# Kernel tuning notes

Hardware: AMD Instinct MI355X
Metric: run time of the kernel (lower is better)

Reference implementation:

```python
import jax, jax.numpy as jnp
import numpy as np

N = 8192
IN_DIM = 512
HID = 512


def setup_inputs() -> dict:
    key = jax.random.key(0)
    k1, k2, k3, k4 = jax.random.split(key, 4)
    input_features = jax.random.normal(k1, (N, IN_DIM), dtype=jnp.float32)
    # positive weighted adjacency so degrees > 0
    adjacency_matrix = jax.random.uniform(k2, (N, N), dtype=jnp.float32)
    # xavier_init: normal with std = 1/sqrt(in_dim/2)
    Wgcn1 = jax.random.normal(k3, (IN_DIM, HID), dtype=jnp.float32) * (1.0 / np.sqrt(IN_DIM / 2.0))
    bgcn1 = jnp.zeros((HID,), dtype=jnp.float32)
    Wgcn12 = jax.random.normal(k4, (HID, HID), dtype=jnp.float32) * (1.0 / np.sqrt(HID / 2.0))
    bgcn12 = jnp.zeros((HID,), dtype=jnp.float32)
    return {
        "input_features": input_features,
        "adjacency_matrix": adjacency_matrix,
        "Wgcn1": Wgcn1,
        "bgcn1": bgcn1,
        "Wgcn12": Wgcn12,
        "bgcn12": bgcn12,
    }


def reference(input_features, adjacency_matrix, Wgcn1, bgcn1, Wgcn12, bgcn12):
    # D^{-1/2} A D^{-1/2}: diag matmuls expressed as row/col elementwise scaling
    # (mathematically identical to torch.matmul(diag(d), A @ diag(d)))
    d_inv_sqrt = jnp.power(adjacency_matrix.sum(axis=1), -0.5)  # [N]
    norm_adj = d_inv_sqrt[:, None] * adjacency_matrix * d_inv_sqrt[None, :]  # [N, N]

    support = input_features @ Wgcn1            # [N, HID]
    out = norm_adj @ support + bgcn1            # [N, HID]
    out = jax.nn.relu(out)                      # dropout p=0.0 -> identity
    support = out @ Wgcn12                      # [N, HID]
    out = norm_adj @ support + bgcn12           # [N, HID]
    return out
```

## Files before the change

### kernel.cpp

```cpp
#include <hip/hip_runtime.h>
#include <stdint.h>


typedef __attribute__((ext_vector_type(8))) __bf16 bf16x8;
typedef __attribute__((ext_vector_type(4))) float f32x4;
typedef __attribute__((ext_vector_type(8))) unsigned short u16x8;

__device__ __forceinline__ unsigned short f2bf(float f) {
  union { float f; uint32_t u; } v; v.f = f;
  uint32_t u = v.u;
  return (unsigned short)((u + 0x7fffu + ((u >> 16) & 1u)) >> 16);
}

__device__ __forceinline__ float bf2f(unsigned short u) {
  union { uint32_t u; float f; } v; v.u = ((uint32_t)u) << 16; return v.f;
}

__device__ __forceinline__ void async_cp16(const void* g, void* lds) {
  auto gp = (const __attribute__((address_space(1))) uint32_t*)g;
  auto lp = (__attribute__((address_space(3))) uint32_t*)lds;
  __builtin_amdgcn_global_load_lds(gp, lp, 16, 0, 0);
}

__global__ __launch_bounds__(256) void k_rowsum_convert(
    const float* __restrict__ A, unsigned short* __restrict__ Abf,
    float* __restrict__ dvec, int ncols) {
  const int row = blockIdx.x;
  const float* arow = A + (size_t)row * ncols;
  unsigned short* orow = Abf + (size_t)row * ncols;
  float s = 0.f;
  for (int c = threadIdx.x * 4; c < ncols; c += 256 * 4) {
    float4 v = *(const float4*)(arow + c);
    s += (v.x + v.y) + (v.z + v.w);
    ushort4 o;
    o.x = f2bf(v.x); o.y = f2bf(v.y); o.z = f2bf(v.z); o.w = f2bf(v.w);
    *(ushort4*)(orow + c) = o;
  }
  #pragma unroll
  for (int off = 32; off > 0; off >>= 1) s += __shfl_down(s, off);
  __shared__ float red[4];
  if ((threadIdx.x & 63) == 0) red[threadIdx.x >> 6] = s;
  __syncthreads();
  if (threadIdx.x == 0) {
    float t = (red[0] + red[1]) + (red[2] + red[3]);
    dvec[row] = 1.0f / sqrtf(t);
  }
}

__global__ __launch_bounds__(256) void k_f32_to_bf16(
    const float* __restrict__ in, unsigned short* __restrict__ out, int n4) {
  int i = blockIdx.x * 256 + threadIdx.x;
  if (i < n4) {
    float4 v = ((const float4*)in)[i];
    ushort4 o;
    o.x = f2bf(v.x); o.y = f2bf(v.y); o.z = f2bf(v.z); o.w = f2bf(v.w);
    ((ushort4*)out)[i] = o;
  }
}

__global__ __launch_bounds__(256) void k_transpose_bf16(
    const float* __restrict__ in, unsigned short* __restrict__ out, int dim) {
  int o = blockIdx.x * 256 + threadIdx.x;
  if (o < dim * dim) {
    int k = o % dim;
    int n = o / dim;
    out[o] = f2bf(in[k * dim + n]);
  }
}

template <int MODE>
__global__ __launch_bounds__(256, 2) void gemm_bt(
    const unsigned short* __restrict__ Aop,
    const unsigned short* __restrict__ Bt,
    void* __restrict__ Cout,
    const float* __restrict__ dvec,
    const float* __restrict__ bias,
    int M, int N, int K) {
  constexpr int BM = 128, BN = 64, BK = 32;
  __shared__ unsigned short As[BM * BK];
  __shared__ unsigned short Bs[BN * BK];

  const int tid = threadIdx.x;
  const int w = tid >> 6;
  const int l = tid & 63;
  const int rowBase = blockIdx.y * BM;
  const int colBase = blockIdx.x * BN;
  const int waveM = w >> 1;
  const int waveN = w & 1;

  f32x4 acc[4][2];
  const f32x4 fz = {0.f, 0.f, 0.f, 0.f};
  #pragma unroll
  for (int m = 0; m < 4; ++m)
    #pragma unroll
    for (int n = 0; n < 2; ++n) acc[m][n] = fz;

  const int chunkRow = l >> 2;
  const int kOff = (l & 3) * 8;
  const unsigned short* gA0 = Aop + (size_t)(rowBase + w * 16 + chunkRow) * K + kOff;
  const unsigned short* gA1 = gA0 + (size_t)64 * K;
  const unsigned short* gB0 = Bt + (size_t)(colBase + w * 16 + chunkRow) * K + kOff;
  unsigned short* lA0 = As + w * 512;
  unsigned short* lA1 = As + (w + 4) * 512;
  unsigned short* lB0 = Bs + w * 512;

  const int kfrag = (l >> 4) * 8;
  const int lrow = l & 15;

  for (int k0 = 0; k0 < K; k0 += BK) {
    async_cp16(gA0 + k0, lA0);
    async_cp16(gA1 + k0, lA1);
    async_cp16(gB0 + k0, lB0);
    __syncthreads();

    bf16x8 af[4], bfr[2];
    #pragma unroll
    for (int m = 0; m < 4; ++m)
      af[m] = *(const bf16x8*)(As + (waveM * 64 + m * 16 + lrow) * BK + kfrag);
    #pragma unroll
    for (int n = 0; n < 2; ++n)
      bfr[n] = *(const bf16x8*)(Bs + (waveN * 32 + n * 16 + lrow) * BK + kfrag);

    #pragma unroll
    for (int m = 0; m < 4; ++m)
      #pragma unroll
      for (int n = 0; n < 2; ++n)
        acc[m][n] = __builtin_amdgcn_mfma_f32_16x16x32_bf16(af[m], bfr[n],
                                                            acc[m][n], 0, 0, 0);
    __syncthreads();
  }

  const int erow0 = rowBase + waveM * 64 + (l >> 4) * 4;
  const int ecol0 = colBase + waveN * 32 + (l & 15);
  #pragma unroll
  for (int m = 0; m < 4; ++m) {
    #pragma unroll
    for (int n = 0; n < 2; ++n) {
      #pragma unroll
      for (int j = 0; j < 4; ++j) {
        const int rowg = erow0 + m * 16 + j;
        const int colg = ecol0 + n * 16;
        float v = acc[m][n][j];
        if (MODE == 0) {
          v *= dvec[colg];
          ((unsigned short*)Cout)[(size_t)rowg * N + colg] = f2bf(v);
        }
      }
    }
  }
}

__global__ __launch_bounds__(512, 1) void gemm_big3(
    const unsigned short* __restrict__ Aop,
    const unsigned short* __restrict__ Bt,
    unsigned short* __restrict__ Pout,
    int M, int N, int K, int kLen) {
  constexpr int BK = 32;
  __shared__ char lds[3 * 32768];

  const int tid = threadIdx.x;
  const int w = tid >> 6;
  const int l = tid & 63;

  const int id = blockIdx.x;
  const int q = id & 7, s = id >> 3;
  const int bx = s & 1;
  const int by = ((q & 1) << 4) | (s >> 1);
  const int bz = q >> 1;

  const int rowBase = by * 256;
  const int colBase = bx * 256;
  const int kBase = bz * kLen;
  const int waveM = w >> 2;
  const int waveN = w & 3;

  f32x4 acc[8][4];
  const f32x4 fz = {0.f, 0.f, 0.f, 0.f};
  #pragma unroll
  for (int m = 0; m < 8; ++m)
    #pragma unroll
    for (int n = 0; n < 4; ++n) acc[m][n] = fz;

  const int srcElem = ((l & 3) ^ ((l >> 3) & 3)) * 8;
  const unsigned short* aSrc =
      Aop + (size_t)(rowBase + w * 32 + (l >> 2)) * K + kBase + srcElem;
  const unsigned short* bSrc =
      Bt + (size_t)(colBase + w * 32 + (l >> 2)) * K + kBase + srcElem;
  const int dstTh = w * 2048 + l * 16;

#define STAGE_A(tt, bb)                                                   \
  {                                                                       \
    const size_t o = (size_t)(tt) * BK;                                   \
    async_cp16(aSrc + o, lds + (bb) + dstTh);                             \
    async_cp16(aSrc + (size_t)16 * K + o, lds + (bb) + dstTh + 1024);     \
  }
#define STAGE_B(tt, bb)                                                   \
  {                                                                       \
    const size_t o = (size_t)(tt) * BK;                                   \
    async_cp16(bSrc + o, lds + (bb) + 16384 + dstTh);                     \
    async_cp16(bSrc + (size_t)16 * K + o, lds + (bb) + 16384 + dstTh + 1024); \
  }

  const int nt = kLen / BK;
  STAGE_A(0, 0); STAGE_B(0, 0);
  STAGE_A(1, 32768); STAGE_B(1, 32768);

  const int lrow = l & 15;
  const int kq = l >> 4;
  const int xr = (lrow >> 1) & 3;
  const int slotByte = ((kq ^ xr) << 4);
  const int aRow0 = (waveM * 128 + lrow) * 64;
  const int bRow0 = 16384 + (waveN * 64 + lrow) * 64;

  int cur = 0, nxt = 32768, fut = 65536;
  for (int t = 0; t < nt; ++t) {
    if (t == nt - 1) {
      asm volatile("s_waitcnt vmcnt(0)" ::: "memory");
    } else {
      asm volatile("s_waitcnt vmcnt(4)" ::: "memory");
    }
    __builtin_amdgcn_s_barrier();

    bf16x8 af[4], bfr[4];
    #pragma unroll
    for (int i = 0; i < 4; ++i)
      af[i] = *(const bf16x8*)(lds + cur + aRow0 + i * 16 * 64 + slotByte);
    #pragma unroll
    for (int n = 0; n < 4; ++n)
      bfr[n] = *(const bf16x8*)(lds + cur + bRow0 + n * 16 * 64 + slotByte);
    if (t + 2 < nt) STAGE_A(t + 2, fut);
    __builtin_amdgcn_s_barrier();
    __builtin_amdgcn_s_setprio(1);
    #pragma unroll
    for (int i = 0; i < 4; ++i)
      #pragma unroll
      for (int n = 0; n < 4; ++n)
        acc[i][n] = __builtin_amdgcn_mfma_f32_16x16x32_bf16(
            af[i], bfr[n], acc[i][n], 0, 0, 0);
    __builtin_amdgcn_s_setprio(0);

    bf16x8 af2[4];
    #pragma unroll
    for (int i = 0; i < 4; ++i)
      af2[i] = *(const bf16x8*)(lds + cur + aRow0 + (64 + i * 16) * 64 + slotByte);
    if (t + 2 < nt) STAGE_B(t + 2, fut);
    __builtin_amdgcn_s_barrier();
    __builtin_amdgcn_s_setprio(1);
    #pragma unroll
    for (int i = 0; i < 4; ++i)
      #pragma unroll
      for (int n = 0; n < 4; ++n)
        acc[4 + i][n] = __builtin_amdgcn_mfma_f32_16x16x32_bf16(
            af2[i], bfr[n], acc[4 + i][n], 0, 0, 0);
    __builtin_amdgcn_s_setprio(0);

    const int tmp = cur; cur = nxt; nxt = fut; fut = tmp;
  }
#undef STAGE_A
#undef STAGE_B

  unsigned short* pz = Pout + (size_t)bz * M * N;
  const int erow0 = rowBase + waveM * 128 + (l >> 4) * 4;
  const int ecol0 = colBase + waveN * 64 + (l & 15);
  #pragma unroll
  for (int m = 0; m < 8; ++m) {
    #pragma unroll
    for (int n = 0; n < 4; ++n) {
      #pragma unroll
      for (int j = 0; j < 4; ++j) {
        pz[(size_t)(erow0 + m * 16 + j) * N + ecol0 + n * 16] =
            f2bf(acc[m][n][j]);
      }
    }
  }
}

template <int MODE>
__global__ __launch_bounds__(256) void k_reduce(
    const unsigned short* __restrict__ parts,
    const float* __restrict__ dvec,
    const float* __restrict__ bias,
    void* __restrict__ outp, int M, int N) {
  const size_t MN = (size_t)M * N;
  const size_t idx = ((size_t)blockIdx.x * 256 + threadIdx.x) * 8;
  if (idx >= MN) return;
  const int row = (int)(idx / N);
  const int col = (int)(idx % N);
  const float di = dvec[row];
  float s[8] = {0, 0, 0, 0, 0, 0, 0, 0};
  #pragma unroll
  for (int z = 0; z < 4; ++z) {
    u16x8 v = *(const u16x8*)(parts + z * MN + idx);
    #pragma unroll
    for (int e = 0; e < 8; ++e) s[e] += bf2f(v[e]);
  }
  if (MODE == 1) {
    ushort4 o0, o1;
    unsigned short tmp[8];
    #pragma unroll
    for (int e = 0; e < 8; ++e) {
      float v = di * s[e] + bias[col + e];
      v = v > 0.f ? v : 0.f;
      tmp[e] = f2bf(v);
    }
    o0.x = tmp[0]; o0.y = tmp[1]; o0.z = tmp[2]; o0.w = tmp[3];
    o1.x = tmp[4]; o1.y = tmp[5]; o1.z = tmp[6]; o1.w = tmp[7];
    *(ushort4*)((unsigned short*)outp + idx) = o0;
    *(ushort4*)((unsigned short*)outp + idx + 4) = o1;
  } else {
    float4 o0, o1;
    o0.x = di * s[0] + bias[col + 0];
    o0.y = di * s[1] + bias[col + 1];
    o0.z = di * s[2] + bias[col + 2];
    o0.w = di * s[3] + bias[col + 3];
    o1.x = di * s[4] + bias[col + 4];
    o1.y = di * s[5] + bias[col + 5];
    o1.z = di * s[6] + bias[col + 6];
    o1.w = di * s[7] + bias[col + 7];
    *(float4*)((float*)outp + idx) = o0;
    *(float4*)((float*)outp + idx + 4) = o1;
  }
}

extern "C" void kernel_launch(void* const* d_in, const int* in_sizes, int n_in,
                              void* d_out, int out_size, void* d_ws, size_t ws_size,
                              hipStream_t stream) {
  const float* X  = (const float*)d_in[0];
  const float* A  = (const float*)d_in[1];
  const float* W1 = (const float*)d_in[2];
  const float* b1 = (const float*)d_in[3];
  const float* W2 = (const float*)d_in[4];
  const float* b2 = (const float*)d_in[5];
  float* out = (float*)d_out;

  constexpr int NN = 8192, IN = 512, HID = 512;
  constexpr int KSPLIT = 4;

  char* ws = (char*)d_ws;
  float* ddeg = (float*)ws;
  unsigned short* Abf = (unsigned short*)(ws + (32 << 10));
  unsigned short* W1t = Abf + (size_t)NN * NN;
  unsigned short* W2t = W1t + IN * HID;
  unsigned short* P0  = W2t + HID * HID;
  unsigned short* P1  = P0 + (size_t)NN * HID;
  unsigned short* parts = P1 + (size_t)NN * HID;

  k_rowsum_convert<<<NN, 256, 0, stream>>>(A, Abf, ddeg, NN);
  k_f32_to_bf16<<<(NN * IN / 4 + 255) / 256, 256, 0, stream>>>(X, P0, NN * IN / 4);
  k_transpose_bf16<<<(IN * HID + 255) / 256, 256, 0, stream>>>(W1, W1t, IN);
  k_transpose_bf16<<<(HID * HID + 255) / 256, 256, 0, stream>>>(W2, W2t, HID);

  gemm_bt<0><<<dim3(NN / 64, HID / 128), 256, 0, stream>>>(
      W1t, P0, P1, ddeg, nullptr, HID, NN, IN);
  gemm_big3<<<2 * (NN / 256) * KSPLIT, 512, 0, stream>>>(
      Abf, P1, parts, NN, HID, NN, NN / KSPLIT);
  k_reduce<1><<<(int)((size_t)NN * HID / 8 / 256), 256, 0, stream>>>(
      parts, ddeg, b1, P0, NN, HID);
  gemm_bt<0><<<dim3(NN / 64, HID / 128), 256, 0, stream>>>(
      W2t, P0, P1, ddeg, nullptr, HID, NN, HID);
  gemm_big3<<<2 * (NN / 256) * KSPLIT, 512, 0, stream>>>(
      Abf, P1, parts, NN, HID, NN, NN / KSPLIT);
  k_reduce<2><<<(int)((size_t)NN * HID / 8 / 256), 256, 0, stream>>>(
      parts, ddeg, b2, out, NN, HID);
}
```

Measured before the change: 263.3 us.

## Rewrite big GEMM mainloop with BK=64 double buffer and phased staggered prefetch

Replaces the triple-buffered BK=32 main loop of the split-K adjacency GEMM with a double-buffered BK=64 loop using 128 KB LDS and an 8-way XOR swizzle. Each K-tile is split into four MFMA phases separated by barriers. The A and B prefetches are staggered so A for the next tile and B for the tile after next are issued across different phases. The aim is to halve the barrier and wait overhead per unit of K and overlap global-to-LDS copies with MFMA work. In exchange it adds more barriers per iteration and depends on fragile vmcnt accounting. The launch bound also changes to 2, while 128 KB of LDS per block still likely allows only one block per CU.

```diff
diff --git a/kernel.cpp b/kernel.cpp
--- a/kernel.cpp
+++ b/kernel.cpp
@@ -150,13 +150,12 @@
   }
 }
 
-__global__ __launch_bounds__(512, 1) void gemm_big3(
+__global__ __launch_bounds__(512, 2) void gemm_big8p(
     const unsigned short* __restrict__ Aop,
     const unsigned short* __restrict__ Bt,
     unsigned short* __restrict__ Pout,
     int M, int N, int K, int kLen) {
-  constexpr int BK = 32;
-  __shared__ char lds[3 * 32768];
+  __shared__ char lds[131072];
 
   const int tid = threadIdx.x;
   const int w = tid >> 6;
@@ -181,83 +180,130 @@
     #pragma unroll
     for (int n = 0; n < 4; ++n) acc[m][n] = fz;
 
-  const int srcElem = ((l & 3) ^ ((l >> 3) & 3)) * 8;
+  const int srcSwz = ((l & 7) ^ ((l >> 3) & 7)) * 8;
   const unsigned short* aSrc =
-      Aop + (size_t)(rowBase + w * 32 + (l >> 2)) * K + kBase + srcElem;
+      Aop + (size_t)(rowBase + w * 8 + (l >> 3)) * K + kBase + srcSwz;
   const unsigned short* bSrc =
-      Bt + (size_t)(colBase + w * 32 + (l >> 2)) * K + kBase + srcElem;
-  const int dstTh = w * 2048 + l * 16;
-
-#define STAGE_A(tt, bb)                                                   \
-  {                                                                       \
-    const size_t o = (size_t)(tt) * BK;                                   \
-    async_cp16(aSrc + o, lds + (bb) + dstTh);                             \
-    async_cp16(aSrc + (size_t)16 * K + o, lds + (bb) + dstTh + 1024);     \
-  }
-#define STAGE_B(tt, bb)                                                   \
-  {                                                                       \
-    const size_t o = (size_t)(tt) * BK;                                   \
-    async_cp16(bSrc + o, lds + (bb) + 16384 + dstTh);                     \
-    async_cp16(bSrc + (size_t)16 * K + o, lds + (bb) + 16384 + dstTh + 1024); \
-  }
-
-  const int nt = kLen / BK;
-  STAGE_A(0, 0); STAGE_B(0, 0);
-  STAGE_A(1, 32768); STAGE_B(1, 32768);
+      Bt + (size_t)(colBase + w * 8 + (l >> 3)) * K + kBase + srcSwz;
+  const int dstTh = w * 1024 + l * 16;
+
+#define STG_A(i, tt, bb) \
+  async_cp16(aSrc + (size_t)(i) * 64 * K + (size_t)(tt) * 64, \
+             lds + (bb) + (i) * 8192 + dstTh)
+#define STG_B(i, tt, bb) \
+  async_cp16(bSrc + (size_t)(i) * 64 * K + (size_t)(tt) * 64, \
+             lds + (bb) + 32768 + (i) * 8192 + dstTh)
+
+  const int nt = kLen / 64;
+  STG_A(0, 0, 0); STG_A(2, 0, 0); STG_A(1, 0, 0); STG_A(3, 0, 0);
+  STG_B(0, 0, 0); STG_B(1, 0, 0); STG_B(2, 0, 0); STG_B(3, 0, 0);
+  STG_A(0, 1, 65536); STG_A(2, 1, 65536); STG_A(1, 1, 65536); STG_A(3, 1, 65536);
+  STG_B(0, 1, 65536); STG_B(1, 1, 65536); STG_B(2, 1, 65536); STG_B(3, 1, 65536);
+  asm volatile("s_waitcnt vmcnt(8)" ::: "memory");
+  __builtin_amdgcn_s_barrier();
 
   const int lrow = l & 15;
   const int kq = l >> 4;
-  const int xr = (lrow >> 1) & 3;
-  const int slotByte = ((kq ^ xr) << 4);
-  const int aRow0 = (waveM * 128 + lrow) * 64;
-  const int bRow0 = 16384 + (waveN * 64 + lrow) * 64;
-
-  int cur = 0, nxt = 32768, fut = 65536;
+  const int swz7 = l & 7;
+  const int aRow0 = (waveM * 128 + lrow) * 128;
+  const int bRow0 = 32768 + (waveN * 64 + lrow) * 128;
+  const int slot0 = ((kq ^ swz7) << 4);
+  const int slot1 = (((4 + kq) ^ swz7) << 4);
+
   for (int t = 0; t < nt; ++t) {
-    if (t == nt - 1) {
-      asm volatile("s_waitcnt vmcnt(0)" ::: "memory");
-    } else {
-      asm volatile("s_waitcnt vmcnt(4)" ::: "memory");
-    }
-    __builtin_amdgcn_s_barrier();
-
-    bf16x8 af[4], bfr[4];
-    #pragma unroll
-    for (int i = 0; i < 4; ++i)
-      af[i] = *(const bf16x8*)(lds + cur + aRow0 + i * 16 * 64 + slotByte);
+    const int base = (t & 1) << 16;
+    const int obase = base ^ 65536;
+    const char* Ab = lds + base;
+    const char* Bb = lds + base;
+    const bool stgA = (t + 1 < nt);
+    const bool stgB = (t + 2 < nt);
+
+    bf16x8 af0[4], bf0[4];
+    #pragma unroll
+    for (int i = 0; i < 4; ++i)
+      af0[i] = *(const bf16x8*)(Ab + aRow0 + i * 16 * 128 + slot0);
     #pragma unroll
     for (int n = 0; n < 4; ++n)
-      bfr[n] = *(const bf16x8*)(lds + cur + bRow0 + n * 16 * 64 + slotByte);
-    if (t + 2 < nt) STAGE_A(t + 2, fut);
-    __builtin_amdgcn_s_barrier();
+      bf0[n] = *(const bf16x8*)(Bb + bRow0 + n * 16 * 128 + slot0);
+    if (stgA && t >= 1) { STG_A(0, t + 1, obase); STG_A(2, t + 1, obase); }
+    __builtin_amdgcn_sched_barrier(0);
+    __builtin_amdgcn_s_barrier();
+    asm volatile("s_waitcnt lgkmcnt(0)" ::: "memory");
+    __builtin_amdgcn_sched_barrier(0);
     __builtin_amdgcn_s_setprio(1);
     #pragma unroll
     for (int i = 0; i < 4; ++i)
       #pragma unroll
       for (int n = 0; n < 4; ++n)
         acc[i][n] = __builtin_amdgcn_mfma_f32_16x16x32_bf16(
-            af[i], bfr[n], acc[i][n], 0, 0, 0);
+            af0[i], bf0[n], acc[i][n], 0, 0, 0);
     __builtin_amdgcn_s_setprio(0);
-
-    bf16x8 af2[4];
-    #pragma unroll
-    for (int i = 0; i < 4; ++i)
-      af2[i] = *(const bf16x8*)(lds + cur + aRow0 + (64 + i * 16) * 64 + slotByte);
-    if (t + 2 < nt) STAGE_B(t + 2, fut);
-    __builtin_amdgcn_s_barrier();
+    __builtin_amdgcn_s_barrier();
+
+    bf16x8 af1[4];
+    #pragma unroll
+    for (int i = 0; i < 4; ++i)
+      af1[i] = *(const bf16x8*)(Ab + aRow0 + (64 + i * 16) * 128 + slot0);
+    if (stgA && t >= 1) { STG_A(1, t + 1, obase); STG_A(3, t + 1, obase); }
+    __builtin_amdgcn_sched_barrier(0);
+    __builtin_amdgcn_s_barrier();
+    asm volatile("s_waitcnt lgkmcnt(0)" ::: "memory");
+    __builtin_amdgcn_sched_barrier(0);
     __builtin_amdgcn_s_setprio(1);
     #pragma unroll
     for (int i = 0; i < 4; ++i)
       #pragma unroll
       for (int n = 0; n < 4; ++n)
         acc[4 + i][n] = __builtin_amdgcn_mfma_f32_16x16x32_bf16(
-            af2[i], bfr[n], acc[4 + i][n], 0, 0, 0);
+            af1[i], bf0[n], acc[4 + i][n], 0, 0, 0);
     __builtin_amdgcn_s_setprio(0);
-
-    const int tmp = cur; cur = nxt; nxt = fut; fut = tmp;
-  }
-#undef STAGE_A
-#undef STAGE_B
+    __builtin_amdgcn_s_barrier();
+
+    bf16x8 af2_[4], bf1[4];
+    #pragma unroll
+    for (int i = 0; i < 4; ++i)
+      af2_[i] = *(const bf16x8*)(Ab + aRow0 + i * 16 * 128 + slot1);
+    #pragma unroll
+    for (int n = 0; n < 4; ++n)
+      bf1[n] = *(const bf16x8*)(Bb + bRow0 + n * 16 * 128 + slot1);
+    __builtin_amdgcn_sched_barrier(0);
+    __builtin_amdgcn_s_barrier();
+    asm volatile("s_waitcnt lgkmcnt(0)" ::: "memory");
+    __builtin_amdgcn_sched_barrier(0);
+    __builtin_amdgcn_s_setprio(1);
+    #pragma unroll
+    for (int i = 0; i < 4; ++i)
+      #pragma unroll
+      for (int n = 0; n < 4; ++n)
+        acc[i][n] = __builtin_amdgcn_mfma_f32_16x16x32_bf16(
+            af2_[i], bf1[n], acc[i][n], 0, 0, 0);
+    __builtin_amdgcn_s_setprio(0);
+    __builtin_amdgcn_s_barrier();
+
+    bf16x8 af3[4];
+    #pragma unroll
+    for (int i = 0; i < 4; ++i)
+      af3[i] = *(const bf16x8*)(Ab + aRow0 + (64 + i * 16) * 128 + slot1);
+    if (stgB) { STG_B(0, t + 2, base); STG_B(1, t + 2, base);
+                STG_B(2, t + 2, base); STG_B(3, t + 2, base); }
+    __builtin_amdgcn_sched_barrier(0);
+    if (stgB) { asm volatile("s_waitcnt vmcnt(4)" ::: "memory"); }
+    else      { asm volatile("s_waitcnt vmcnt(0)" ::: "memory"); }
+    __builtin_amdgcn_s_barrier();
+    asm volatile("s_waitcnt lgkmcnt(0)" ::: "memory");
+    __builtin_amdgcn_sched_barrier(0);
+    __builtin_amdgcn_s_setprio(1);
+    #pragma unroll
+    for (int i = 0; i < 4; ++i)
+      #pragma unroll
+      for (int n = 0; n < 4; ++n)
+        acc[4 + i][n] = __builtin_amdgcn_mfma_f32_16x16x32_bf16(
+            af3[i], bf1[n], acc[4 + i][n], 0, 0, 0);
+    __builtin_amdgcn_s_setprio(0);
+    __builtin_amdgcn_s_barrier();
+  }
+#undef STG_A
+#undef STG_B
 
   unsigned short* pz = Pout + (size_t)bz * M * N;
   const int erow0 = rowBase + waveM * 128 + (l >> 4) * 4;
@@ -352,13 +398,13 @@
 
   gemm_bt<0><<<dim3(NN / 64, HID / 128), 256, 0, stream>>>(
       W1t, P0, P1, ddeg, nullptr, HID, NN, IN);
-  gemm_big3<<<2 * (NN / 256) * KSPLIT, 512, 0, stream>>>(
+  gemm_big8p<<<2 * (NN / 256) * KSPLIT, 512, 0, stream>>>(
       Abf, P1, parts, NN, HID, NN, NN / KSPLIT);
   k_reduce<1><<<(int)((size_t)NN * HID / 8 / 256), 256, 0, stream>>>(
       parts, ddeg, b1, P0, NN, HID);
   gemm_bt<0><<<dim3(NN / 64, HID / 128), 256, 0, stream>>>(
       W2t, P0, P1, ddeg, nullptr, HID, NN, HID);
-  gemm_big3<<<2 * (NN / 256) * KSPLIT, 512, 0, stream>>>(
+  gemm_big8p<<<2 * (NN / 256) * KSPLIT, 512, 0, stream>>>(
       Abf, P1, parts, NN, HID, NN, NN / KSPLIT);
   k_reduce<2><<<(int)((size_t)NN * HID / 8 / 256), 256, 0, stream>>>(
       parts, ddeg, b2, out, NN, HID);
```

After: 265.8 us. About the same (+1.0%).
